# Performance work log

Measured on AMD Instinct MI355X. Metric: run time of the kernel, lower is better.

Reference implementation:

```python
import jax, jax.numpy as jnp
import numpy as np
import math

VOCAB, E, CTX, DK, DH, H, HID, L = 50257, 768, 2048, 64, 64, 12, 3072, 2
B, S = 2, 2048
NEG_INF = -1e30


def _pos_encoding(seq_len, dim):
    pos = jnp.arange(seq_len, dtype=jnp.float32)[:, None]
    i = jnp.arange(dim, dtype=jnp.float32)[None, :]
    angle = pos / jnp.power(10000.0, 2.0 * i / dim)
    return jnp.where(jnp.arange(dim)[None, :] % 2 == 0, jnp.sin(angle), jnp.cos(angle))


def _layernorm(x, scale, bias, eps=1e-5):
    mu = jnp.mean(x, axis=-1, keepdims=True)
    var = jnp.var(x, axis=-1, keepdims=True)
    return (x - mu) * jax.lax.rsqrt(var + eps) * scale + bias


def setup_inputs() -> dict:
    key = jax.random.key(0)
    ks = jax.random.split(key, 10)
    s = 0.02  # init scale for stability
    return {
        "tokens": jax.random.randint(ks[0], (B, S), 0, VOCAB),
        "emb": jax.random.normal(ks[1], (VOCAB, E), jnp.float32) * s,
        "ln1_s": jnp.ones((L, E), jnp.float32),
        "ln1_b": jnp.zeros((L, E), jnp.float32),
        "Wq": jax.random.normal(ks[2], (L, H, E, DK), jnp.float32) * s,
        "bq": jnp.zeros((L, H, DK), jnp.float32),
        "Wk": jax.random.normal(ks[3], (L, H, E, DK), jnp.float32) * s,
        "bk": jnp.zeros((L, H, DK), jnp.float32),
        "Wv": jax.random.normal(ks[4], (L, H, E, DH), jnp.float32) * s,
        "bv": jnp.zeros((L, H, DH), jnp.float32),
        "ln2_s": jnp.ones((L, E), jnp.float32),
        "ln2_b": jnp.zeros((L, E), jnp.float32),
        "W1": jax.random.normal(ks[5], (L, E, HID), jnp.float32) * s,
        "b1": jnp.zeros((L, HID), jnp.float32),
        "W2": jax.random.normal(ks[6], (L, HID, E), jnp.float32) * s,
        "b2": jnp.zeros((L, E), jnp.float32),
        "Wout": jax.random.normal(ks[7], (E, VOCAB), jnp.float32) * s,
        "bout": jnp.zeros((VOCAB,), jnp.float32),
    }


def reference(tokens, emb, ln1_s, ln1_b, Wq, bq, Wk, bk, Wv, bv, ln2_s, ln2_b, W1, b1, W2, b2, Wout, bout):
    seq = tokens.shape[1]
    x = emb[tokens] + _pos_encoding(seq, E)  # [B,S,E]
    causal = jnp.triu(jnp.full((seq, seq), NEG_INF, jnp.float32), k=1)
    for l in range(Wq.shape[0]):
        # pre-norm on attention input; note residual adds to the NORMALIZED h (faithful to original)
        h = _layernorm(x, ln1_s[l], ln1_b[l])
        q = jnp.einsum('bse,hed->bhsd', h, Wq[l]) + bq[l][None, :, None, :]
        k = jnp.einsum('bse,hed->bhsd', h, Wk[l]) + bk[l][None, :, None, :]
        v = jnp.einsum('bse,hed->bhsd', h, Wv[l]) + bv[l][None, :, None, :]
        scores = jnp.einsum('bhsd,bhtd->bhst', q, k) / math.sqrt(DK) + causal
        w = jax.nn.softmax(scores, axis=-1)  # [B,H,S,S]
        o = jnp.einsum('bhst,bhtd->bhsd', w, v)  # [B,H,S,DH]
        o = jnp.transpose(o, (0, 2, 1, 3)).reshape(o.shape[0], seq, H * DH)  # concat heads
        x = h + o
        h2 = _layernorm(x, ln2_s[l], ln2_b[l])
        x = h2 + jnp.einsum('bsf,fe->bse', jax.nn.relu(jnp.einsum('bse,ef->bsf', h2, W1[l]) + b1[l]), W2[l]) + b2[l]
    logits = jnp.einsum('bse,ev->bsv', x, Wout) + bout  # training-mode output
    return logits
```

## Files before the change

kernel.cpp:

```cpp
#include <hip/hip_runtime.h>
#include <stdint.h>

#define DEV static __device__ __forceinline__

typedef unsigned short u16;
typedef __attribute__((ext_vector_type(8))) short short8;
typedef __attribute__((ext_vector_type(4))) float f32x4;

#define B_     2
#define S_     2048
#define E_     768
#define H_     12
#define L_     2
#define HID_   3072
#define VOCAB_ 50257
#define VPAD_  50432
#define M_     4096
#define NQKV_  2304

DEV u16 f2bf(float f) {
  union { float f; unsigned u; } x; x.f = f;
  unsigned r = x.u + 0x7fffu + ((x.u >> 16) & 1u);
  return (u16)(r >> 16);
}

DEV void gload16(const void* g, void* lds) {
  __builtin_amdgcn_global_load_lds(
      (const __attribute__((address_space(1))) unsigned int*)g,
      (__attribute__((address_space(3))) unsigned int*)lds, 16, 0, 0);
}

__global__ __launch_bounds__(256) void k_transp(
    const float* __restrict__ in, u16* __restrict__ out,
    int R, int Cin, long long ib1, long long ib2, long long ob1, long long ob2, int zdiv)
{
  __shared__ float t[32][33];
  const int z = blockIdx.z;
  const float* ib = in  + (size_t)(z / zdiv) * ib1 + (size_t)(z % zdiv) * ib2;
  u16*         ob = out + (size_t)(z / zdiv) * ob1 + (size_t)(z % zdiv) * ob2;
  const int c0 = blockIdx.x * 32, r0 = blockIdx.y * 32;
  const int tx = threadIdx.x, ty = threadIdx.y;
#pragma unroll
  for (int i = 0; i < 4; i++) {
    const int c = c0 + tx, r = r0 + ty + i * 8;
    t[ty + i * 8][tx] = (c < Cin) ? ib[(size_t)r * Cin + c] : 0.f;
  }
  __syncthreads();
#pragma unroll
  for (int i = 0; i < 4; i++) {
    const int orow = c0 + ty + i * 8;
    ob[(size_t)orow * R + r0 + tx] = f2bf(t[tx][ty + i * 8]);
  }
}

__global__ __launch_bounds__(256) void k_pack_bias(
    const float* __restrict__ bq, const float* __restrict__ bk,
    const float* __restrict__ bv, float* __restrict__ bqkv)
{
  const int i = blockIdx.x * 256 + threadIdx.x;
  if (i >= L_ * NQKV_) return;
  const int l = i / NQKV_, n = i % NQKV_;
  const float* s = (n < 768) ? bq : (n < 1536) ? bk : bv;
  bqkv[i] = s[l * 768 + (n % 768)];
}

__global__ __launch_bounds__(256) void k_embed(
    const int* __restrict__ tok, const float* __restrict__ emb, float* __restrict__ x)
{
  const int idx = blockIdx.x * 256 + threadIdx.x;
  const int e = idx % E_;
  const int row = idx / E_;
  const int s = row & (S_ - 1);
  const int t = tok[row];
  const float ang = (float)s * expf((float)e * (-2.0f / 768.f) * 9.210340371976184f);
  const float pe = (e & 1) ? cosf(ang) : sinf(ang);
  x[idx] = emb[(size_t)t * E_ + e] + pe;
}

__global__ __launch_bounds__(256) void k_ln(
    const float* __restrict__ xin, const float* __restrict__ sc,
    const float* __restrict__ bi, float* __restrict__ hout, u16* __restrict__ hb)
{
  const int row  = blockIdx.x * 4 + (threadIdx.x >> 6);
  const int lane = threadIdx.x & 63;
  const float* xr = xin + (size_t)row * E_;
  float v[12];
  float s = 0.f;
#pragma unroll
  for (int i = 0; i < 12; i++) { v[i] = xr[i * 64 + lane]; s += v[i]; }
#pragma unroll
  for (int o = 1; o < 64; o <<= 1) s += __shfl_xor(s, o);
  const float mu = s * (1.f / 768.f);
  float s2 = 0.f;
#pragma unroll
  for (int i = 0; i < 12; i++) { const float d = v[i] - mu; s2 += d * d; }
#pragma unroll
  for (int o = 1; o < 64; o <<= 1) s2 += __shfl_xor(s2, o);
  const float rs = rsqrtf(s2 * (1.f / 768.f) + 1e-5f);
#pragma unroll
  for (int i = 0; i < 12; i++) {
    const int c = i * 64 + lane;
    const float ov = (v[i] - mu) * rs * sc[c] + bi[c];
    hout[(size_t)row * E_ + c] = ov;
    hb[(size_t)row * E_ + c]   = f2bf(ov);
  }
}

template <int EPI>
__global__ __launch_bounds__(256) void k_gemm(
    const u16* __restrict__ A, const u16* __restrict__ Bt,
    const float* __restrict__ bias, const float* __restrict__ res,
    void* __restrict__ outp, u16* __restrict__ out2, int Mm, int Nn, int Kk)
{
  __shared__ __align__(16) u16 As[128 * 32];
  __shared__ __align__(16) u16 Bs[128 * 32];
  const int tid  = threadIdx.x;
  const int lane = tid & 63;
  const int wid  = tid >> 6;
  const int wr = wid >> 1, wc = wid & 1;
  const int m0 = blockIdx.y * 128, n0 = blockIdx.x * 128;

  const u16* Ab = A  + (size_t)m0 * Kk;
  const u16* Bb = Bt + (size_t)n0 * Kk;

  f32x4 acc[4][4];
#pragma unroll
  for (int i = 0; i < 4; i++)
#pragma unroll
    for (int j = 0; j < 4; j++) acc[i][j] = (f32x4){0.f, 0.f, 0.f, 0.f};

  const int c0 = tid, c1 = 256 + tid;
  const int a0row = c0 >> 2, a0k = (c0 & 3) * 8;
  const int a1row = c1 >> 2, a1k = (c1 & 3) * 8;
  const int nk = Kk >> 5;
  const int kg = (lane >> 4) * 8;
  const int arow = wr * 64 + (lane & 15);
  const int brow = wc * 64 + (lane & 15);

  for (int kt = 0; kt < nk; ++kt) {
    const int kof = kt * 32;
    __syncthreads();
    gload16(Ab + (size_t)a0row * Kk + kof + a0k, &As[c0 * 8]);
    gload16(Ab + (size_t)a1row * Kk + kof + a1k, &As[c1 * 8]);
    gload16(Bb + (size_t)a0row * Kk + kof + a0k, &Bs[c0 * 8]);
    gload16(Bb + (size_t)a1row * Kk + kof + a1k, &Bs[c1 * 8]);
    asm volatile("s_waitcnt vmcnt(0)" ::: "memory");
    __syncthreads();
    short8 af[4], bf[4];
#pragma unroll
    for (int i = 0; i < 4; i++) af[i] = *(const short8*)&As[(arow + i * 16) * 32 + kg];
#pragma unroll
    for (int i = 0; i < 4; i++) bf[i] = *(const short8*)&Bs[(brow + i * 16) * 32 + kg];
#pragma unroll
    for (int mi = 0; mi < 4; mi++)
#pragma unroll
      for (int ni = 0; ni < 4; ni++)
        acc[mi][ni] = __builtin_amdgcn_mfma_f32_16x16x32_bf16(af[mi], bf[ni], acc[mi][ni], 0, 0, 0);
  }

  const int colg = lane & 15;
  const int rowg = (lane >> 4) * 4;
#pragma unroll
  for (int mi = 0; mi < 4; mi++) {
#pragma unroll
    for (int ni = 0; ni < 4; ni++) {
      const int col = n0 + wc * 64 + ni * 16 + colg;
      const float bb = bias[col];
#pragma unroll
      for (int r = 0; r < 4; r++) {
        const int row = m0 + wr * 64 + mi * 16 + rowg + r;
        float v = acc[mi][ni][r] + bb;
        if (EPI == 0)      ((u16*)outp)[(size_t)row * Nn + col] = f2bf(v);
        else if (EPI == 1) ((u16*)outp)[(size_t)row * Nn + col] = f2bf(fmaxf(v, 0.f));
        else if (EPI == 2) ((float*)outp)[(size_t)row * Nn + col] = v + res[(size_t)row * Nn + col];
        else if (EPI == 4) {
          const float o = v + res[(size_t)row * Nn + col];
          ((float*)outp)[(size_t)row * Nn + col] = o;
          out2[(size_t)row * Nn + col] = f2bf(o);
        }
      }
    }
  }
}

__global__ __launch_bounds__(512, 2) void k_gemm256(
    const u16* __restrict__ A, const u16* __restrict__ Bt,
    const float* __restrict__ bias, float* __restrict__ out,
    int Nn, int Kk, int nreal, int mpx)
{
  __shared__ __align__(16) u16 As[2][256 * 64];
  __shared__ __align__(16) u16 Bs[2][256 * 64];

  const int id = blockIdx.x;
  const int xcd = id & 7;
  const int j = id >> 3;
  const int m0 = (xcd * mpx + (j % mpx)) * 256;
  const int n0 = (j / mpx) * 256;

  const int tid = threadIdx.x, lane = tid & 63, w = tid >> 6;
  const int wr = w >> 2, wcn = w & 3;
  const int l15 = lane & 15, ks = lane >> 4;

  const u16* Ab = A  + (size_t)m0 * Kk;
  const u16* Bb = Bt + (size_t)n0 * Kk;

  const int srow  = lane >> 3;
  const int sslot = ((lane & 7) ^ srow) * 8;
  const int wrow  = w * 8;

  f32x4 acc[8][4];
#pragma unroll
  for (int i = 0; i < 8; i++)
#pragma unroll
    for (int n = 0; n < 4; n++) acc[i][n] = (f32x4){0.f, 0.f, 0.f, 0.f};

  const int nk = Kk >> 6;

  auto stA = [&](int b, int R, int ko) {
    gload16(Ab + (size_t)(R + wrow + srow) * Kk + ko + sslot,      &As[b][(R + wrow) * 64]);
    gload16(Ab + (size_t)(R + 64 + wrow + srow) * Kk + ko + sslot, &As[b][(R + 64 + wrow) * 64]);
  };
  auto stB = [&](int b, int R, int ko) {
    gload16(Bb + (size_t)(R + wrow + srow) * Kk + ko + sslot,      &Bs[b][(R + wrow) * 64]);
    gload16(Bb + (size_t)(R + 64 + wrow + srow) * Kk + ko + sslot, &Bs[b][(R + 64 + wrow) * 64]);
  };

  short8 af[4], bf[4];
  auto ldA = [&](int b, int fmh, int ksub) {
#pragma unroll
    for (int i = 0; i < 4; i++) {
      const int r = wr * 128 + fmh * 64 + i * 16 + l15;
      const int sl = ((ksub * 4 + ks) ^ (r & 7)) * 8;
      af[i] = *(const short8*)&As[b][r * 64 + sl];
    }
  };
  auto ldB = [&](int b, int ksub) {
#pragma unroll
    for (int n = 0; n < 4; n++) {
      const int r = wcn * 64 + n * 16 + l15;
      const int sl = ((ksub * 4 + ks) ^ (r & 7)) * 8;
      bf[n] = *(const short8*)&Bs[b][r * 64 + sl];
    }
  };
  auto mm = [&](int fmh) {
    __builtin_amdgcn_s_setprio(1);
#pragma unroll
    for (int i = 0; i < 4; i++)
#pragma unroll
      for (int n = 0; n < 4; n++)
        acc[fmh * 4 + i][n] =
            __builtin_amdgcn_mfma_f32_16x16x32_bf16(af[i], bf[n], acc[fmh * 4 + i][n], 0, 0, 0);
    __builtin_amdgcn_s_setprio(0);
  };

#define BAR_() do { __builtin_amdgcn_sched_barrier(0); __builtin_amdgcn_s_barrier(); \
                    __builtin_amdgcn_sched_barrier(0); } while (0)
#define LGKM_() do { asm volatile("s_waitcnt lgkmcnt(0)" ::: "memory"); \
                     __builtin_amdgcn_sched_barrier(0); } while (0)

  stA(0, 0, 0); stA(0, 128, 0); stB(0, 0, 0); stB(0, 128, 0);
  if (nk > 1) {
    stA(1, 0, 64); stA(1, 128, 64);
    asm volatile("s_waitcnt vmcnt(4)" ::: "memory");
  } else {
    asm volatile("s_waitcnt vmcnt(0)" ::: "memory");
  }
  BAR_();

  for (int t = 0; t < nk; ++t) {
    const int cur = t & 1;
    const int kon = (t + 1) << 6;
    ldA(cur, 0, 0); ldB(cur, 0);
    if (t + 1 < nk) stB(cur ^ 1, 0, kon);
    BAR_(); LGKM_(); mm(0); BAR_();
    ldA(cur, 1, 0);
    if (t + 1 < nk) stB(cur ^ 1, 128, kon);
    BAR_(); LGKM_(); mm(1); BAR_();
    ldA(cur, 0, 1); ldB(cur, 1);
    BAR_(); LGKM_(); mm(0); BAR_();
    ldA(cur, 1, 1);
    BAR_(); LGKM_(); mm(1); BAR_();
    if (t + 2 < nk) {
      const int kon2 = (t + 2) << 6;
      stA(cur, 0, kon2); stA(cur, 128, kon2);
      asm volatile("s_waitcnt vmcnt(4)" ::: "memory");
    } else {
      asm volatile("s_waitcnt vmcnt(0)" ::: "memory");
    }
    BAR_();
  }
#undef BAR_
#undef LGKM_

#pragma unroll
  for (int fm = 0; fm < 8; fm++) {
    const int row = m0 + wr * 128 + fm * 16 + ks * 4;
#pragma unroll
    for (int n = 0; n < 4; n++) {
      const int col = n0 + wcn * 64 + n * 16 + l15;
      if (col < nreal) {
        const float bb = bias[col];
#pragma unroll
        for (int r = 0; r < 4; r++)
          out[(size_t)(row + r) * nreal + col] = acc[fm][n][r] + bb;
      }
    }
  }
}

__global__ __launch_bounds__(256) void k_attn(
    const u16* __restrict__ qkv, const float* __restrict__ h, float* __restrict__ x)
{
  const int tid = threadIdx.x, lane = tid & 63, wid = tid >> 6;
  const int bh = blockIdx.y, b = bh / H_, hh = bh % H_;
  const int q0 = blockIdx.x * 64;
  const int qw = q0 + wid * 16;

  __shared__ __align__(16) u16 Ks[128 * 72];
  __shared__ __align__(16) u16 Vt[64 * 136];
  __shared__ __align__(16) u16 Ps[4][16 * 136];

  const size_t rowbase = (size_t)b * S_;
  const u16* qb = qkv + rowbase * NQKV_ + hh * 64;
  const u16* kb = qb + 768;
  const u16* vb = qb + 1536;

  const int l15 = lane & 15;
  const int ks  = lane >> 4;
  const int kg  = ks * 8;
  const int ks4 = ks * 4;

  short8 qf0, qf1;
  {
    const u16* g = qb + (size_t)(qw + l15) * NQKV_ + kg;
    qf0 = *(const short8*)g;
    qf1 = *(const short8*)(g + 32);
  }

  f32x4 ov[4];
#pragma unroll
  for (int i = 0; i < 4; i++) ov[i] = (f32x4){0.f, 0.f, 0.f, 0.f};
  float mr[4], lr[4];
#pragma unroll
  for (int r = 0; r < 4; r++) { mr[r] = -1e30f; lr[r] = 0.f; }

  const int srow = tid >> 3;
  const int sc8  = (tid & 7) * 8;
  const int g8   = tid & 7;
  const int nkt  = (q0 >> 7) + 1;

  for (int kt = 0; kt < nkt; ++kt) {
    const int kbase = kt << 7;
    __syncthreads();
#pragma unroll
    for (int pass = 0; pass < 4; ++pass) {
      const int r = srow + pass * 32;
      const size_t gr = (size_t)(kbase + r) * NQKV_;
      const uint4 kd = *(const uint4*)(kb + gr + sc8);
      *(uint4*)&Ks[r * 72 + sc8] = kd;
      const uint4 vd = *(const uint4*)(vb + gr + sc8);
      const u16* ve = (const u16*)&vd;
      const int sb = (((r >> 3) ^ g8) << 3) + (r & 7);
#pragma unroll
      for (int jj = 0; jj < 8; jj++) Vt[(sc8 + jj) * 136 + sb] = ve[jj];
    }
    __syncthreads();

    const bool last = (kt == nkt - 1);
    float p[8][4], mt[4];
#pragma unroll
    for (int r = 0; r < 4; r++) mt[r] = -1e30f;
#pragma unroll
    for (int ct = 0; ct < 8; ++ct) {
      f32x4 s = (f32x4){0.f, 0.f, 0.f, 0.f};
      const short8 kf0 = *(const short8*)&Ks[(ct * 16 + l15) * 72 + kg];
      const short8 kf1 = *(const short8*)&Ks[(ct * 16 + l15) * 72 + 32 + kg];
      s = __builtin_amdgcn_mfma_f32_16x16x32_bf16(qf0, kf0, s, 0, 0, 0);
      s = __builtin_amdgcn_mfma_f32_16x16x32_bf16(qf1, kf1, s, 0, 0, 0);
      const int kc = kbase + ct * 16 + l15;
#pragma unroll
      for (int r = 0; r < 4; r++) {
        float v = s[r] * 0.125f;
        if (last && kc > qw + ks4 + r) v = -1e30f;
        p[ct][r] = v;
        mt[r] = fmaxf(mt[r], v);
      }
    }
#pragma unroll
    for (int r = 0; r < 4; r++) {
#pragma unroll
      for (int off = 1; off < 16; off <<= 1) mt[r] = fmaxf(mt[r], __shfl_xor(mt[r], off));
    }
    float al[4], ps[4];
#pragma unroll
    for (int r = 0; r < 4; r++) {
      const float mn = fmaxf(mr[r], mt[r]);
      al[r] = __expf(mr[r] - mn);
      mr[r] = mn;
      ps[r] = 0.f;
    }
#pragma unroll
    for (int ct = 0; ct < 8; ++ct)
#pragma unroll
      for (int r = 0; r < 4; r++) {
        p[ct][r] = __expf(p[ct][r] - mr[r]);
        ps[r] += p[ct][r];
      }
#pragma unroll
    for (int r = 0; r < 4; r++) {
#pragma unroll
      for (int off = 1; off < 16; off <<= 1) ps[r] += __shfl_xor(ps[r], off);
      lr[r] = lr[r] * al[r] + ps[r];
    }
#pragma unroll
    for (int dt = 0; dt < 4; dt++)
#pragma unroll
      for (int r = 0; r < 4; r++) ov[dt][r] *= al[r];

    u16* pw = &Ps[wid][0];
#pragma unroll
    for (int ct = 0; ct < 8; ++ct)
#pragma unroll
      for (int r = 0; r < 4; r++)
        pw[(ks4 + r) * 136 + ct * 16 + l15] = f2bf(p[ct][r]);
#pragma unroll
    for (int c = 0; c < 4; ++c) {
      const short8 pa = *(const short8*)&pw[l15 * 136 + c * 32 + kg];
#pragma unroll
      for (int dt = 0; dt < 4; dt++) {
        const int d = dt * 16 + l15;
        const int sb = (((c * 4 + ks) ^ ((d >> 3) & 7)) << 3);
        const short8 vf = *(const short8*)&Vt[d * 136 + sb];
        ov[dt] = __builtin_amdgcn_mfma_f32_16x16x32_bf16(pa, vf, ov[dt], 0, 0, 0);
      }
    }
  }

#pragma unroll
  for (int dt = 0; dt < 4; dt++) {
#pragma unroll
    for (int r = 0; r < 4; r++) {
      const int qr = qw + ks4 + r;
      const int col = hh * 64 + dt * 16 + l15;
      const size_t idx = (rowbase + qr) * (size_t)E_ + col;
      x[idx] = h[idx] + ov[dt][r] / lr[r];
    }
  }
}

extern "C" void kernel_launch(void* const* d_in, const int* in_sizes, int n_in,
                              void* d_out, int out_size, void* d_ws, size_t ws_size,
                              hipStream_t stream)
{
  const int*   tok  = (const int*)  d_in[0];
  const float* emb  = (const float*)d_in[1];
  const float* ln1s = (const float*)d_in[2];
  const float* ln1b = (const float*)d_in[3];
  const float* Wq   = (const float*)d_in[4];
  const float* bq   = (const float*)d_in[5];
  const float* Wk   = (const float*)d_in[6];
  const float* bk   = (const float*)d_in[7];
  const float* Wv   = (const float*)d_in[8];
  const float* bv   = (const float*)d_in[9];
  const float* ln2s = (const float*)d_in[10];
  const float* ln2b = (const float*)d_in[11];
  const float* W1   = (const float*)d_in[12];
  const float* b1   = (const float*)d_in[13];
  const float* W2   = (const float*)d_in[14];
  const float* b2   = (const float*)d_in[15];
  const float* Wo   = (const float*)d_in[16];
  const float* bo   = (const float*)d_in[17];
  float* out = (float*)d_out;

  char* p = (char*)d_ws;
  float* xf    = (float*)p; p += (size_t)M_ * E_ * 4;
  float* hf    = (float*)p; p += (size_t)M_ * E_ * 4;
  u16*   hb    = (u16*)p;   p += (size_t)M_ * E_ * 2;
  u16*   xb    = (u16*)p;   p += (size_t)M_ * E_ * 2;
  u16*   midb  = (u16*)p;   p += (size_t)M_ * HID_ * 2;
  u16*   qkvb  = (u16*)p;   p += (size_t)M_ * NQKV_ * 2;
  u16*   Wqkvt = (u16*)p;   p += (size_t)L_ * NQKV_ * E_ * 2;
  u16*   W1t   = (u16*)p;   p += (size_t)L_ * HID_ * E_ * 2;
  u16*   W2t   = (u16*)p;   p += (size_t)L_ * E_ * HID_ * 2;
  u16*   Wot   = (u16*)p;   p += (size_t)VPAD_ * E_ * 2;
  float* bqkv  = (float*)p; p += (size_t)L_ * NQKV_ * 4;

  const dim3 tb32(32, 8, 1);
  k_transp<<<dim3(HID_ / 32, E_ / 32, L_), tb32, 0, stream>>>(
      W1, W1t, E_, HID_, (long long)E_ * HID_, 0, (long long)HID_ * E_, 0, 1);
  k_transp<<<dim3(E_ / 32, HID_ / 32, L_), tb32, 0, stream>>>(
      W2, W2t, HID_, E_, (long long)HID_ * E_, 0, (long long)E_ * HID_, 0, 1);
  k_transp<<<dim3(VPAD_ / 32, E_ / 32, 1), tb32, 0, stream>>>(
      Wo, Wot, E_, VOCAB_, 0, 0, 0, 0, 1);
  k_transp<<<dim3(2, E_ / 32, L_ * H_), tb32, 0, stream>>>(
      Wq, Wqkvt, E_, 64, (long long)H_ * E_ * 64, (long long)E_ * 64,
      (long long)NQKV_ * E_, 64LL * E_, H_);
  k_transp<<<dim3(2, E_ / 32, L_ * H_), tb32, 0, stream>>>(
      Wk, Wqkvt + 768 * E_, E_, 64, (long long)H_ * E_ * 64, (long long)E_ * 64,
      (long long)NQKV_ * E_, 64LL * E_, H_);
  k_transp<<<dim3(2, E_ / 32, L_ * H_), tb32, 0, stream>>>(
      Wv, Wqkvt + 1536 * E_, E_, 64, (long long)H_ * E_ * 64, (long long)E_ * 64,
      (long long)NQKV_ * E_, 64LL * E_, H_);
  k_pack_bias<<<18, 256, 0, stream>>>(bq, bk, bv, bqkv);
  k_embed<<<(M_ * E_) / 256, 256, 0, stream>>>(tok, emb, xf);

  for (int l = 0; l < L_; ++l) {
    k_ln<<<M_ / 4, 256, 0, stream>>>(xf, ln1s + l * E_, ln1b + l * E_, hf, hb);
    k_gemm<0><<<dim3(NQKV_ / 128, M_ / 128), 256, 0, stream>>>(
        hb, Wqkvt + (size_t)l * NQKV_ * E_, bqkv + l * NQKV_, nullptr, qkvb, nullptr,
        M_, NQKV_, E_);
    k_attn<<<dim3(S_ / 64, B_ * H_), 256, 0, stream>>>(qkvb, hf, xf);
    k_ln<<<M_ / 4, 256, 0, stream>>>(xf, ln2s + l * E_, ln2b + l * E_, hf, hb);
    k_gemm<1><<<dim3(HID_ / 128, M_ / 128), 256, 0, stream>>>(
        hb, W1t + (size_t)l * HID_ * E_, b1 + l * HID_, nullptr, midb, nullptr,
        M_, HID_, E_);
    if (l == L_ - 1) {
      k_gemm<4><<<dim3(E_ / 128, M_ / 128), 256, 0, stream>>>(
          midb, W2t + (size_t)l * E_ * HID_, b2 + l * E_, hf, xf, xb, M_, E_, HID_);
    } else {
      k_gemm<2><<<dim3(E_ / 128, M_ / 128), 256, 0, stream>>>(
          midb, W2t + (size_t)l * E_ * HID_, b2 + l * E_, hf, xf, nullptr, M_, E_, HID_);
    }
  }
  k_gemm256<<<dim3(8 * 2 * (VPAD_ / 256)), 512, 0, stream>>>(
      xb, Wot, bo, out, VPAD_, E_, VOCAB_, 2);
}
```

Before: 1.187 ms.

## Simplify GEMM main loop to plain double buffering with two barriers per k-step

Replaces the interleaved ping-pong schedule, which split A/B staging across sub-phases with many barriers and explicit lgkmcnt waits, with a simpler double-buffered loop. Each iteration issues all LDS reads and MFMAs for the current buffer, syncs, then prefetches the whole A and B tile for k+2 into the freed buffer. This cuts barrier and waitcnt overhead and lets the compiler schedule LDS loads and MFMAs freely, but it loses the explicit overlap of global loads with compute and may expose more memory latency.

```diff
diff --git a/kernel.cpp b/kernel.cpp
--- a/kernel.cpp
+++ b/kernel.cpp
@@ -216,13 +216,15 @@
 
   const int nk = Kk >> 6;
 
-  auto stA = [&](int b, int R, int ko) {
-    gload16(Ab + (size_t)(R + wrow + srow) * Kk + ko + sslot,      &As[b][(R + wrow) * 64]);
-    gload16(Ab + (size_t)(R + 64 + wrow + srow) * Kk + ko + sslot, &As[b][(R + 64 + wrow) * 64]);
-  };
-  auto stB = [&](int b, int R, int ko) {
-    gload16(Bb + (size_t)(R + wrow + srow) * Kk + ko + sslot,      &Bs[b][(R + wrow) * 64]);
-    gload16(Bb + (size_t)(R + 64 + wrow + srow) * Kk + ko + sslot, &Bs[b][(R + 64 + wrow) * 64]);
+  auto stage = [&](int b, int ko) {
+    gload16(Ab + (size_t)(wrow + srow) * Kk + ko + sslot,       &As[b][wrow * 64]);
+    gload16(Ab + (size_t)(64 + wrow + srow) * Kk + ko + sslot,  &As[b][(64 + wrow) * 64]);
+    gload16(Ab + (size_t)(128 + wrow + srow) * Kk + ko + sslot, &As[b][(128 + wrow) * 64]);
+    gload16(Ab + (size_t)(192 + wrow + srow) * Kk + ko + sslot, &As[b][(192 + wrow) * 64]);
+    gload16(Bb + (size_t)(wrow + srow) * Kk + ko + sslot,       &Bs[b][wrow * 64]);
+    gload16(Bb + (size_t)(64 + wrow + srow) * Kk + ko + sslot,  &Bs[b][(64 + wrow) * 64]);
+    gload16(Bb + (size_t)(128 + wrow + srow) * Kk + ko + sslot, &Bs[b][(128 + wrow) * 64]);
+    gload16(Bb + (size_t)(192 + wrow + srow) * Kk + ko + sslot, &Bs[b][(192 + wrow) * 64]);
   };
 
   short8 af[4], bf[4];
@@ -253,44 +255,34 @@
     __builtin_amdgcn_s_setprio(0);
   };
 
-#define BAR_() do { __builtin_amdgcn_sched_barrier(0); __builtin_amdgcn_s_barrier(); \
-                    __builtin_amdgcn_sched_barrier(0); } while (0)
-#define LGKM_() do { asm volatile("s_waitcnt lgkmcnt(0)" ::: "memory"); \
-                     __builtin_amdgcn_sched_barrier(0); } while (0)
-
-  stA(0, 0, 0); stA(0, 128, 0); stB(0, 0, 0); stB(0, 128, 0);
+  stage(0, 0);
   if (nk > 1) {
-    stA(1, 0, 64); stA(1, 128, 64);
-    asm volatile("s_waitcnt vmcnt(4)" ::: "memory");
+    stage(1, 64);
+    asm volatile("s_waitcnt vmcnt(8)" ::: "memory");
   } else {
     asm volatile("s_waitcnt vmcnt(0)" ::: "memory");
   }
-  BAR_();
+  __builtin_amdgcn_s_barrier();
 
   for (int t = 0; t < nk; ++t) {
     const int cur = t & 1;
-    const int kon = (t + 1) << 6;
-    ldA(cur, 0, 0); ldB(cur, 0);
-    if (t + 1 < nk) stB(cur ^ 1, 0, kon);
-    BAR_(); LGKM_(); mm(0); BAR_();
-    ldA(cur, 1, 0);
-    if (t + 1 < nk) stB(cur ^ 1, 128, kon);
-    BAR_(); LGKM_(); mm(1); BAR_();
-    ldA(cur, 0, 1); ldB(cur, 1);
-    BAR_(); LGKM_(); mm(0); BAR_();
-    ldA(cur, 1, 1);
-    BAR_(); LGKM_(); mm(1); BAR_();
+    ldA(cur, 0, 0); ldB(cur, 0); mm(0);
+    ldA(cur, 1, 0); mm(1);
+    ldA(cur, 0, 1); ldB(cur, 1); mm(0);
+    ldA(cur, 1, 1); mm(1);
+    __builtin_amdgcn_sched_barrier(0);
+    __builtin_amdgcn_s_barrier();
+    __builtin_amdgcn_sched_barrier(0);
     if (t + 2 < nk) {
-      const int kon2 = (t + 2) << 6;
-      stA(cur, 0, kon2); stA(cur, 128, kon2);
-      asm volatile("s_waitcnt vmcnt(4)" ::: "memory");
-    } else {
+      stage(cur, (t + 2) << 6);
+      asm volatile("s_waitcnt vmcnt(8)" ::: "memory");
+    } else if (t + 1 < nk) {
       asm volatile("s_waitcnt vmcnt(0)" ::: "memory");
     }
-    BAR_();
-  }
-#undef BAR_
-#undef LGKM_
+    __builtin_amdgcn_sched_barrier(0);
+    __builtin_amdgcn_s_barrier();
+    __builtin_amdgcn_sched_barrier(0);
+  }
 
 #pragma unroll
   for (int fm = 0; fm < 8; fm++) {
```

Result: no change. 1.186 ms (-0.2%).
